# Performance work log

Measured on AMD Instinct MI355X. Metric: run time of the kernel, lower is better.

Reference implementation:

```python
import jax, jax.numpy as jnp
import numpy as np
from jax import lax

B, H, W, C = 8, 64, 64, 256
OUT = 1024          # channels (final conv filters)
KS = 3              # kernel_size
GROUP_DIV = 1
N_GROUPS = C // GROUP_DIV  # 256 -> depthwise-style grouped convs
DN = ('NHWC', 'HWIO', 'NHWC')
EPS = 1e-5


def setup_inputs() -> dict:
    key = jax.random.key(0)
    ks = jax.random.split(key, 6)
    x = jax.random.normal(ks[0], (B, H, W, C), jnp.float32)
    w_spatial = jax.random.normal(ks[1], (B, KS, KS, C // N_GROUPS, C), jnp.float32) * 0.05
    w_pointwise = jax.random.normal(ks[2], (B, 1, 1, C // N_GROUPS, C), jnp.float32) * 0.05
    bias = jax.random.normal(ks[3], (B, C), jnp.float32) * 0.05
    conv_w = jax.random.normal(ks[4], (KS, KS, C, OUT), jnp.float32) * (1.0 / np.sqrt(KS * KS * C))
    conv_b = jnp.zeros((OUT,), jnp.float32)
    return {"x": x, "w_spatial": w_spatial, "w_pointwise": w_pointwise,
            "bias": bias, "conv_w": conv_w, "conv_b": conv_b}


def _instance_norm(x):
    # TF: (x - mean) / (std + eps), population std over H,W per sample/channel
    mean = jnp.mean(x, axis=(1, 2), keepdims=True)
    std = jnp.sqrt(jnp.mean((x - mean) ** 2, axis=(1, 2), keepdims=True))
    return (x - mean) / (std + EPS)


def _per_sample(xi, ws, wp, b):
    # xi: [H,W,C]; ws: [ks,ks,1,C]; wp: [1,1,1,C]; b: [C]
    y = lax.conv_general_dilated(xi[None], ws, (1, 1), 'SAME',
                                 dimension_numbers=DN,
                                 feature_group_count=N_GROUPS)
    y = lax.conv_general_dilated(y, wp, (1, 1), 'VALID',
                                 dimension_numbers=DN,
                                 feature_group_count=N_GROUPS) + b
    return y[0]


def reference(x, w_spatial, w_pointwise, bias, conv_w, conv_b):
    x = _instance_norm(x)
    # batched per-sample dynamic grouped spatial + pointwise conv
    x = jax.vmap(_per_sample)(x, w_spatial, w_pointwise, bias)  # [B,H,W,C]
    # shared 3x3 SAME conv C -> OUT with bias
    y = lax.conv_general_dilated(x, conv_w, (1, 1), 'SAME',
                                 dimension_numbers=DN) + conv_b
    return y
```

## Files before the change

### kernel.cpp

```cpp
#include <hip/hip_runtime.h>
#include <hip/hip_bf16.h>
#include <cstdint>
#include <cstddef>

constexpr int Bn   = 8;
constexpr int Hn   = 64;
constexpr int Wn   = 64;
constexpr int Cn   = 256;
constexpr int OUTC = 1024;
constexpr int HPAD = 66;
constexpr int WPAD = 66;
#define EPS 1e-5f

typedef __attribute__((ext_vector_type(4))) float f32x4;
typedef __bf16 bf16x8 __attribute__((ext_vector_type(8)));

__device__ __forceinline__ void gload_lds16(const void* g, void* l) {
    __builtin_amdgcn_global_load_lds(
        (__attribute__((address_space(1))) void*)g,
        (__attribute__((address_space(3))) void*)l,
        16, 0, 0);
}

__global__ __launch_bounds__(256) void k0_transpose_w(const float* __restrict__ conv_w,
                                                      __hip_bfloat16* __restrict__ wT) {
    __shared__ float tile[64][65];
    const int tap = blockIdx.x;
    const int ct  = blockIdx.y;
    const int ot  = blockIdx.z;
    const int t   = threadIdx.x;
    const int lo  = t & 63;
    const int cq  = t >> 6;

#pragma unroll
    for (int k = 0; k < 16; ++k) {
        int ci = k * 4 + cq;
        tile[lo][ci] = conv_w[((size_t)(tap * Cn + ct * 64 + ci)) * OUTC + ot * 64 + lo];
    }
    __syncthreads();
#pragma unroll
    for (int k = 0; k < 16; ++k) {
        int oo = k * 4 + cq;
        wT[((size_t)(tap * OUTC + ot * 64 + oo)) * Cn + ct * 64 + lo] =
            __float2bfloat16(tile[oo][lo]);
    }
}

__global__ __launch_bounds__(1024) void k1_stats_partial(const float* __restrict__ x,
                                                         float* __restrict__ ps,
                                                         float* __restrict__ pq) {
    __shared__ float sb[2][4][256];
    const int bh = blockIdx.x;
    const int tid = threadIdx.x;
    const int c = tid & 255;
    const int s = tid >> 8;
    const float* row = x + (size_t)bh * Wn * Cn + (size_t)s * 16 * Cn + c;
    float sm = 0.f, q = 0.f;
#pragma unroll
    for (int w = 0; w < 16; ++w) {
        float v = row[(size_t)w * Cn];
        sm += v; q += v * v;
    }
    sb[0][s][c] = sm; sb[1][s][c] = q;
    __syncthreads();
    if (s == 0) {
        float S = 0.f, Q = 0.f;
#pragma unroll
        for (int k = 0; k < 4; ++k) { S += sb[0][k][c]; Q += sb[1][k][c]; }
        ps[bh * Cn + c] = S;
        pq[bh * Cn + c] = Q;
    }
}

__global__ __launch_bounds__(1024) void k2_stats_final(const float* __restrict__ ps,
                                                       const float* __restrict__ pq,
                                                       float* __restrict__ scale,
                                                       float* __restrict__ shift) {
    __shared__ float sb[2][4][256];
    const int b = blockIdx.x;
    const int tid = threadIdx.x;
    const int c = tid & 255;
    const int qd = tid >> 8;
    float S = 0.f, Q = 0.f;
#pragma unroll 4
    for (int i = 0; i < 16; ++i) {
        int h = qd * 16 + i;
        S += ps[(b * Hn + h) * Cn + c];
        Q += pq[(b * Hn + h) * Cn + c];
    }
    sb[0][qd][c] = S; sb[1][qd][c] = Q;
    __syncthreads();
    if (qd == 0) {
        float s2 = 0.f, q2 = 0.f;
#pragma unroll
        for (int k = 0; k < 4; ++k) { s2 += sb[0][k][c]; q2 += sb[1][k][c]; }
        const float inv = 1.f / (float)(Hn * Wn);
        float mean = s2 * inv;
        float var  = fmaxf(q2 * inv - mean * mean, 0.f);
        float sc   = 1.f / (sqrtf(var) + EPS);
        scale[b * Cn + c] = sc;
        shift[b * Cn + c] = -mean * sc;
    }
}

__global__ __launch_bounds__(256) void k3_dwconv(const float* __restrict__ x,
                                                 const float* __restrict__ w_sp,
                                                 const float* __restrict__ w_pw,
                                                 const float* __restrict__ bias,
                                                 const float* __restrict__ scale,
                                                 const float* __restrict__ shift,
                                                 __hip_bfloat16* __restrict__ tpad) {
    const int bq = blockIdx.x;
    const int wq = bq & 3;
    const int bh = bq >> 2;
    const int b  = bh / HPAD;
    const int hp = bh - b * HPAD;
    const int c  = threadIdx.x;
    __hip_bfloat16* orow = tpad + ((size_t)(b * HPAD + hp)) * WPAD * Cn + c;
    const __hip_bfloat16 z = __float2bfloat16(0.f);

    if (hp == 0 || hp == HPAD - 1) {
        int wlo = wq * 17, whi = wlo + 17 < WPAD ? wlo + 17 : WPAD;
        for (int wp = wlo; wp < whi; ++wp) orow[(size_t)wp * Cn] = z;
        return;
    }
    const int h = hp - 1;
    const float sc = scale[b * Cn + c];
    const float sh = shift[b * Cn + c];
    float w9[9];
#pragma unroll
    for (int k = 0; k < 9; ++k) w9[k] = w_sp[(b * 9 + k) * Cn + c];
    const float pw = w_pw[b * Cn + c];
    const float bv = bias[b * Cn + c];
    const float* xb = x + (size_t)b * Hn * Wn * Cn + c;

    bool rv[3];
#pragma unroll
    for (int r = 0; r < 3; ++r) { int rr = h - 1 + r; rv[r] = (rr >= 0 && rr < Hn); }

    if (wq == 0) orow[0] = z;
    if (wq == 3) orow[(size_t)(WPAD - 1) * Cn] = z;

    const int w0 = wq * 16;
    float win[3][3];
#pragma unroll
    for (int r = 0; r < 3; ++r) {
        win[r][0] = (rv[r] && w0 > 0)
                    ? (xb[((size_t)(h - 1 + r) * Wn + (w0 - 1)) * Cn] * sc + sh) : 0.f;
        win[r][1] = rv[r] ? (xb[((size_t)(h - 1 + r) * Wn + w0) * Cn] * sc + sh) : 0.f;
    }
    for (int i = 0; i < 16; ++i) {
        const int w = w0 + i;
#pragma unroll
        for (int r = 0; r < 3; ++r)
            win[r][2] = (rv[r] && (w + 1) < Wn)
                        ? (xb[((size_t)(h - 1 + r) * Wn + (w + 1)) * Cn] * sc + sh) : 0.f;
        float y = 0.f;
#pragma unroll
        for (int r = 0; r < 3; ++r)
#pragma unroll
            for (int qq = 0; qq < 3; ++qq)
                y += win[r][qq] * w9[r * 3 + qq];
        orow[(size_t)(w + 1) * Cn] = __float2bfloat16(y * pw + bv);
#pragma unroll
        for (int r = 0; r < 3; ++r) { win[r][0] = win[r][1]; win[r][1] = win[r][2]; }
    }
}

constexpr int KSTEPS = 36;
constexpr int BUFSZ  = 49152;

__global__ __launch_bounds__(512, 2) void k4_gemm(const __hip_bfloat16* __restrict__ tpad,
                                                  const __hip_bfloat16* __restrict__ wT,
                                                  const float* __restrict__ conv_b,
                                                  float* __restrict__ out) {
    __shared__ __align__(16) char smem[3 * BUFSZ];

    const int tid  = threadIdx.x;
    const int lane = tid & 63;
    const int wv   = tid >> 6;
    const int wm   = wv >> 2;
    const int wn   = wv & 3;
    const int g    = lane >> 4, l15 = lane & 15;

    const int bid = blockIdx.x;
    const int mt  = (bid & 7) * 16 + ((bid >> 3) & 15);
    const int nt  = bid >> 7;
    const int pixbase = mt * 256;
    const int b       = pixbase >> 12;
    const int hbase   = (pixbase & 4095) >> 6;
    const int obase   = nt * 128;

    int a_base[4];
#pragma unroll
    for (int hh = 0; hh < 2; ++hh)
#pragma unroll
        for (int j = 0; j < 2; ++j) {
            int u    = hh * 1024 + j * 512 + tid;
            int grow = u >> 3;
            int sg   = (u & 7) ^ (grow & 7);
            int h    = hbase + (grow >> 6);
            int w    = grow & 63;
            a_base[hh * 2 + j] = ((b * HPAD + h) * WPAD + w) * Cn + sg * 8;
        }
    int b_base[2];
#pragma unroll
    for (int j = 0; j < 2; ++j) {
        int u    = j * 512 + tid;
        int grow = u >> 3;
        int sg   = (u & 7) ^ (grow & 7);
        b_base[j] = (obase + grow) * Cn + sg * 8;
    }

    auto stageA = [&](int step, int hh) {
        const int tap = step >> 2, ks = step & 3;
        const int kh = tap / 3, kw = tap - 3 * kh;
        const __hip_bfloat16* src = tpad + (kh * WPAD + kw) * Cn + ks * 64;
        char* base = smem + (step % 3) * BUFSZ;
        gload_lds16(src + a_base[hh * 2 + 0], base + (hh * 1024 + 0   + wv * 64) * 16);
        gload_lds16(src + a_base[hh * 2 + 1], base + (hh * 1024 + 512 + wv * 64) * 16);
    };
    auto stageB = [&](int step) {
        const int tap = step >> 2, ks = step & 3;
        const __hip_bfloat16* src = wT + (size_t)tap * (OUTC * Cn) + ks * 64;
        char* base = smem + (step % 3) * BUFSZ + 32768;
        gload_lds16(src + b_base[0], base + (0   + wv * 64) * 16);
        gload_lds16(src + b_base[1], base + (512 + wv * 64) * 16);
    };

    f32x4 acc[8][2] = {};

    stageA(0, 0); stageA(0, 1); stageB(0);
    stageA(1, 0); stageA(1, 1); stageB(1);
    asm volatile("s_waitcnt vmcnt(6)" ::: "memory");
    __builtin_amdgcn_s_barrier();
    __builtin_amdgcn_sched_barrier(0);

#pragma unroll 1
    for (int t = 0; t < KSTEPS; ++t) {
        char* Ab = smem + (t % 3) * BUFSZ;
        char* Bb = Ab + 32768;
        const bool pf = (t + 2 < KSTEPS);

        bf16x8 bfr[2][2];
        bf16x8 af[4][2];

#pragma unroll
        for (int n = 0; n < 2; ++n)
#pragma unroll
            for (int kh = 0; kh < 2; ++kh) {
                int row = wn * 32 + n * 16 + l15;
                bfr[n][kh] = *(const bf16x8*)(Bb + row * 128 +
                                ((kh * 64 + g * 16) ^ ((row & 7) << 4)));
            }
#pragma unroll
        for (int m = 0; m < 4; ++m)
#pragma unroll
            for (int kh = 0; kh < 2; ++kh) {
                int row = wm * 128 + m * 16 + l15;
                af[m][kh] = *(const bf16x8*)(Ab + row * 128 +
                                ((kh * 64 + g * 16) ^ ((row & 7) << 4)));
            }
        if (pf) stageA(t + 2, 0);
        __builtin_amdgcn_s_barrier();
        __builtin_amdgcn_sched_barrier(0);
        __builtin_amdgcn_s_setprio(1);
#pragma unroll
        for (int m = 0; m < 4; ++m)
#pragma unroll
            for (int n = 0; n < 2; ++n)
#pragma unroll
                for (int kh = 0; kh < 2; ++kh)
                    acc[m][n] = __builtin_amdgcn_mfma_f32_16x16x32_bf16(
                        af[m][kh], bfr[n][kh], acc[m][n], 0, 0, 0);
        __builtin_amdgcn_s_setprio(0);
        __builtin_amdgcn_s_barrier();
        __builtin_amdgcn_sched_barrier(0);

#pragma unroll
        for (int m = 0; m < 4; ++m)
#pragma unroll
            for (int kh = 0; kh < 2; ++kh) {
                int row = wm * 128 + (m + 4) * 16 + l15;
                af[m][kh] = *(const bf16x8*)(Ab + row * 128 +
                                ((kh * 64 + g * 16) ^ ((row & 7) << 4)));
            }
        if (pf) { stageA(t + 2, 1); stageB(t + 2); }
        __builtin_amdgcn_s_barrier();
        __builtin_amdgcn_sched_barrier(0);
        __builtin_amdgcn_s_setprio(1);
#pragma unroll
        for (int m = 0; m < 4; ++m)
#pragma unroll
            for (int n = 0; n < 2; ++n)
#pragma unroll
                for (int kh = 0; kh < 2; ++kh)
                    acc[m + 4][n] = __builtin_amdgcn_mfma_f32_16x16x32_bf16(
                        af[m][kh], bfr[n][kh], acc[m + 4][n], 0, 0, 0);
        __builtin_amdgcn_s_setprio(0);

        if (pf) { asm volatile("s_waitcnt vmcnt(6)" ::: "memory"); }
        else    { asm volatile("s_waitcnt vmcnt(0)" ::: "memory"); }
        __builtin_amdgcn_s_barrier();
        __builtin_amdgcn_sched_barrier(0);
    }

    float cb[2];
#pragma unroll
    for (int n = 0; n < 2; ++n) cb[n] = conv_b[obase + wn * 32 + n * 16 + l15];
#pragma unroll
    for (int m = 0; m < 8; ++m) {
#pragma unroll
        for (int j = 0; j < 4; ++j) {
            int r = pixbase + wm * 128 + m * 16 + g * 4 + j;
            float* orow = out + (size_t)r * OUTC + obase + wn * 32 + l15;
#pragma unroll
            for (int n = 0; n < 2; ++n)
                orow[n * 16] = acc[m][n][j] + cb[n];
        }
    }
}

extern "C" void kernel_launch(void* const* d_in, const int* in_sizes, int n_in,
                              void* d_out, int out_size, void* d_ws, size_t ws_size,
                              hipStream_t stream) {
    const float* x      = (const float*)d_in[0];
    const float* w_sp   = (const float*)d_in[1];
    const float* w_pw   = (const float*)d_in[2];
    const float* bias   = (const float*)d_in[3];
    const float* conv_w = (const float*)d_in[4];
    const float* conv_b = (const float*)d_in[5];
    float* out = (float*)d_out;

    char* ws = (char*)d_ws;
    __hip_bfloat16* wT    = (__hip_bfloat16*)(ws);
    float*          ps    = (float*)(ws + 4718592);
    float*          pq    = (float*)(ws + 4718592 + 524288);
    float*          scale = (float*)(ws + 5767168);
    float*          shift = (float*)(ws + 5775360);
    __hip_bfloat16* tpad  = (__hip_bfloat16*)(ws + 5783552);

    k0_transpose_w<<<dim3(9, 4, 16), 256, 0, stream>>>(conv_w, wT);
    k1_stats_partial<<<Bn * Hn, 1024, 0, stream>>>(x, ps, pq);
    k2_stats_final<<<Bn, 1024, 0, stream>>>(ps, pq, scale, shift);
    k3_dwconv<<<Bn * HPAD * 4, 256, 0, stream>>>(x, w_sp, w_pw, bias, scale, shift, tpad);
    k4_gemm<<<1024, 512, 0, stream>>>(tpad, wT, conv_b, out);
}
```

Baseline: 210.4 us.

## Widen GEMM tile to 256x256 with K=32 steps and padded LDS rows

The implicit-GEMM conv kernel now computes a 256-pixel by 256-output-channel tile per block instead of 256x128, halving the grid and reusing each A tile across twice as many output channels. The K step shrinks from 64 to 32 channels (72 steps), and LDS rows are padded to 80 bytes instead of XOR-swizzled. The load mapping splits five 16-byte loads per thread across A and B, with a duplicated pad slot. This raises accumulator register pressure (32 MFMA tiles per wave) and doubles the number of barriers per output tile, in exchange for less global traffic on A.

```diff
diff --git a/kernel.cpp b/kernel.cpp
--- a/kernel.cpp
+++ b/kernel.cpp
@@ -167,8 +167,9 @@
     }
 }
 
-constexpr int KSTEPS = 36;
-constexpr int BUFSZ  = 49152;
+constexpr int KSTEPS = 72;
+constexpr int AREG   = 20480;
+constexpr int BUFSZ  = 40960;
 
 __global__ __launch_bounds__(512, 2) void k4_gemm(const __hip_bfloat16* __restrict__ tpad,
                                                   const __hip_bfloat16* __restrict__ wT,
@@ -187,135 +188,121 @@
     const int mt  = (bid & 7) * 16 + ((bid >> 3) & 15);
     const int nt  = bid >> 7;
     const int pixbase = mt * 256;
-    const int b       = pixbase >> 12;
-    const int hbase   = (pixbase & 4095) >> 6;
-    const int obase   = nt * 128;
-
-    int a_base[4];
-#pragma unroll
-    for (int hh = 0; hh < 2; ++hh)
-#pragma unroll
-        for (int j = 0; j < 2; ++j) {
-            int u    = hh * 1024 + j * 512 + tid;
-            int grow = u >> 3;
-            int sg   = (u & 7) ^ (grow & 7);
-            int h    = hbase + (grow >> 6);
-            int w    = grow & 63;
-            a_base[hh * 2 + j] = ((b * HPAD + h) * WPAD + w) * Cn + sg * 8;
-        }
-    int b_base[2];
-#pragma unroll
-    for (int j = 0; j < 2; ++j) {
-        int u    = j * 512 + tid;
-        int grow = u >> 3;
-        int sg   = (u & 7) ^ (grow & 7);
-        b_base[j] = (obase + grow) * Cn + sg * 8;
-    }
-
-    auto stageA = [&](int step, int hh) {
-        const int tap = step >> 2, ks = step & 3;
-        const int kh = tap / 3, kw = tap - 3 * kh;
-        const __hip_bfloat16* src = tpad + (kh * WPAD + kw) * Cn + ks * 64;
-        char* base = smem + (step % 3) * BUFSZ;
-        gload_lds16(src + a_base[hh * 2 + 0], base + (hh * 1024 + 0   + wv * 64) * 16);
-        gload_lds16(src + a_base[hh * 2 + 1], base + (hh * 1024 + 512 + wv * 64) * 16);
+    const int b       = mt >> 4;
+    const int hbase   = (mt & 15) * 4;
+    const int obase   = nt * 256;
+
+    int off5[5];
+#pragma unroll
+    for (int j = 0; j < 5; ++j) {
+        int u = j * 512 + tid;
+        if (u < 1280) {
+            int row = u / 5, rs = u - row * 5;
+            int ls  = (rs == 4) ? 0 : rs;
+            int h   = hbase + (row >> 6);
+            int w   = row & 63;
+            off5[j] = ((b * HPAD + h) * WPAD + w) * Cn + ls * 8;
+        } else {
+            int v = u - 1280;
+            int row = v / 5, rs = v - row * 5;
+            int ls  = (rs == 4) ? 0 : rs;
+            off5[j] = (obase + row) * Cn + ls * 8;
+        }
+    }
+
+    auto stageJ = [&](int s, int j0, int j1) {
+        const int tap = s >> 3, ks = s & 7;
+        const int kh  = (tap * 11) >> 5;
+        const int kw  = tap - kh * 3;
+        const __hip_bfloat16* aS = tpad + ((kh * WPAD + kw) * Cn + ks * 32);
+        const __hip_bfloat16* bS = wT + (size_t)tap * (OUTC * Cn) + ks * 32;
+        char* buf = smem + (s % 3) * BUFSZ;
+#pragma unroll
+        for (int j = 0; j < 5; ++j) {
+            if (j < j0 || j > j1) continue;
+            const __hip_bfloat16* src;
+            if (j <= 1)      src = aS + off5[j];
+            else if (j == 2) src = (tid < 256 ? aS : bS) + off5[j];
+            else             src = bS + off5[j];
+            gload_lds16(src, buf + (size_t)(j * 512 + wv * 64) * 16);
+        }
     };
-    auto stageB = [&](int step) {
-        const int tap = step >> 2, ks = step & 3;
-        const __hip_bfloat16* src = wT + (size_t)tap * (OUTC * Cn) + ks * 64;
-        char* base = smem + (step % 3) * BUFSZ + 32768;
-        gload_lds16(src + b_base[0], base + (0   + wv * 64) * 16);
-        gload_lds16(src + b_base[1], base + (512 + wv * 64) * 16);
-    };
-
-    f32x4 acc[8][2] = {};
-
-    stageA(0, 0); stageA(0, 1); stageB(0);
-    stageA(1, 0); stageA(1, 1); stageB(1);
-    asm volatile("s_waitcnt vmcnt(6)" ::: "memory");
+
+    f32x4 acc[8][4] = {};
+
+    stageJ(0, 0, 4);
+    stageJ(1, 0, 4);
+    asm volatile("s_waitcnt vmcnt(5)" ::: "memory");
     __builtin_amdgcn_s_barrier();
     __builtin_amdgcn_sched_barrier(0);
 
 #pragma unroll 1
     for (int t = 0; t < KSTEPS; ++t) {
         char* Ab = smem + (t % 3) * BUFSZ;
-        char* Bb = Ab + 32768;
+        char* Bb = Ab + AREG;
         const bool pf = (t + 2 < KSTEPS);
 
-        bf16x8 bfr[2][2];
-        bf16x8 af[4][2];
-
-#pragma unroll
-        for (int n = 0; n < 2; ++n)
-#pragma unroll
-            for (int kh = 0; kh < 2; ++kh) {
-                int row = wn * 32 + n * 16 + l15;
-                bfr[n][kh] = *(const bf16x8*)(Bb + row * 128 +
-                                ((kh * 64 + g * 16) ^ ((row & 7) << 4)));
-            }
-#pragma unroll
-        for (int m = 0; m < 4; ++m)
-#pragma unroll
-            for (int kh = 0; kh < 2; ++kh) {
-                int row = wm * 128 + m * 16 + l15;
-                af[m][kh] = *(const bf16x8*)(Ab + row * 128 +
-                                ((kh * 64 + g * 16) ^ ((row & 7) << 4)));
-            }
-        if (pf) stageA(t + 2, 0);
+        bf16x8 bfr[4];
+        bf16x8 af[4];
+
+#pragma unroll
+        for (int n = 0; n < 4; ++n) {
+            int row = wn * 64 + n * 16 + l15;
+            bfr[n] = *(const bf16x8*)(Bb + row * 80 + g * 16);
+        }
+#pragma unroll
+        for (int m = 0; m < 4; ++m) {
+            int row = wm * 128 + m * 16 + l15;
+            af[m] = *(const bf16x8*)(Ab + row * 80 + g * 16);
+        }
+        if (pf) stageJ(t + 2, 0, 2);
         __builtin_amdgcn_s_barrier();
         __builtin_amdgcn_sched_barrier(0);
         __builtin_amdgcn_s_setprio(1);
 #pragma unroll
         for (int m = 0; m < 4; ++m)
 #pragma unroll
-            for (int n = 0; n < 2; ++n)
-#pragma unroll
-                for (int kh = 0; kh < 2; ++kh)
-                    acc[m][n] = __builtin_amdgcn_mfma_f32_16x16x32_bf16(
-                        af[m][kh], bfr[n][kh], acc[m][n], 0, 0, 0);
+            for (int n = 0; n < 4; ++n)
+                acc[m][n] = __builtin_amdgcn_mfma_f32_16x16x32_bf16(
+                    af[m], bfr[n], acc[m][n], 0, 0, 0);
         __builtin_amdgcn_s_setprio(0);
         __builtin_amdgcn_s_barrier();
         __builtin_amdgcn_sched_barrier(0);
 
 #pragma unroll
-        for (int m = 0; m < 4; ++m)
-#pragma unroll
-            for (int kh = 0; kh < 2; ++kh) {
-                int row = wm * 128 + (m + 4) * 16 + l15;
-                af[m][kh] = *(const bf16x8*)(Ab + row * 128 +
-                                ((kh * 64 + g * 16) ^ ((row & 7) << 4)));
-            }
-        if (pf) { stageA(t + 2, 1); stageB(t + 2); }
+        for (int m = 0; m < 4; ++m) {
+            int row = wm * 128 + (m + 4) * 16 + l15;
+            af[m] = *(const bf16x8*)(Ab + row * 80 + g * 16);
+        }
+        if (pf) stageJ(t + 2, 3, 4);
         __builtin_amdgcn_s_barrier();
         __builtin_amdgcn_sched_barrier(0);
         __builtin_amdgcn_s_setprio(1);
 #pragma unroll
         for (int m = 0; m < 4; ++m)
 #pragma unroll
-            for (int n = 0; n < 2; ++n)
-#pragma unroll
-                for (int kh = 0; kh < 2; ++kh)
-                    acc[m + 4][n] = __builtin_amdgcn_mfma_f32_16x16x32_bf16(
-                        af[m][kh], bfr[n][kh], acc[m + 4][n], 0, 0, 0);
+            for (int n = 0; n < 4; ++n)
+                acc[m + 4][n] = __builtin_amdgcn_mfma_f32_16x16x32_bf16(
+                    af[m], bfr[n], acc[m + 4][n], 0, 0, 0);
         __builtin_amdgcn_s_setprio(0);
 
-        if (pf) { asm volatile("s_waitcnt vmcnt(6)" ::: "memory"); }
-        else    { asm volatile("s_waitcnt vmcnt(0)" ::: "memory"); }
+        if (pf)                      { asm volatile("s_waitcnt vmcnt(5)" ::: "memory"); }
+        else if (t + 1 < KSTEPS)     { asm volatile("s_waitcnt vmcnt(0)" ::: "memory"); }
         __builtin_amdgcn_s_barrier();
         __builtin_amdgcn_sched_barrier(0);
     }
 
-    float cb[2];
-#pragma unroll
-    for (int n = 0; n < 2; ++n) cb[n] = conv_b[obase + wn * 32 + n * 16 + l15];
+    float cb[4];
+#pragma unroll
+    for (int n = 0; n < 4; ++n) cb[n] = conv_b[obase + wn * 64 + n * 16 + l15];
 #pragma unroll
     for (int m = 0; m < 8; ++m) {
 #pragma unroll
         for (int j = 0; j < 4; ++j) {
             int r = pixbase + wm * 128 + m * 16 + g * 4 + j;
-            float* orow = out + (size_t)r * OUTC + obase + wn * 32 + l15;
-#pragma unroll
-            for (int n = 0; n < 2; ++n)
+            float* orow = out + (size_t)r * OUTC + obase + wn * 64 + l15;
+#pragma unroll
+            for (int n = 0; n < 4; ++n)
                 orow[n * 16] = acc[m][n][j] + cb[n];
         }
     }
@@ -344,5 +331,5 @@
     k1_stats_partial<<<Bn * Hn, 1024, 0, stream>>>(x, ps, pq);
     k2_stats_final<<<Bn, 1024, 0, stream>>>(ps, pq, scale, shift);
     k3_dwconv<<<Bn * HPAD * 4, 256, 0, stream>>>(x, w_sp, w_pw, bias, scale, shift, tpad);
-    k4_gemm<<<1024, 512, 0, stream>>>(tpad, wT, conv_b, out);
-}
+    k4_gemm<<<512, 512, 0, stream>>>(tpad, wT, conv_b, out);
+}
```

Result: faster. 203.6 us (-3.2%).
